# Performance work log

Measured on AMD Instinct MI355X. Metric: run time of the kernel, lower is better.

The kernel has to match this reference:

```python
import jax, jax.numpy as jnp
import numpy as np

# ---- P4M (D4) group: 8 elements, idx = 4*m + r (m: mirror bit, r: rot90 count) ----
G = 8

def _mr(i):
    return i // 4, i % 4

def _gidx(m, r):
    return 4 * (m % 2) + (r % 4)

def _comp(a, b):
    m1, r1 = _mr(a); m2, r2 = _mr(b)
    return _gidx(m1 + m2, (r1 if m2 == 0 else -r1) + r2)

_INV = [next(b for b in range(G) if _comp(a, b) == 0) for a in range(G)]
# _PERM[h, g] = index of h^{-1} * g  (left regular action on the group axis)
_PERM = np.array([[_comp(_INV[h], g) for g in range(G)] for h in range(G)])


def _spatial_transform(K, h):
    # act on the last two (spatial) kernel axes by group element h = mirror^m rot^r
    m, r = _mr(h)
    if m:
        K = jnp.flip(K, axis=-1)
    return jnp.rot90(K, k=r, axes=(-2, -1))


def _transformed_kernels(W):
    # W: [N_out, N_in, G, k, k] -> [G, N_out, N_in, G, k, k], one kernel per output group element
    return jnp.stack([_spatial_transform(W[:, :, _PERM[h]], h) for h in range(G)])


def conv_gg(x, W, padding):
    # group->group convolution. x: [B, N_in, G, H, W]; W: [N_out, N_in, G, k, k]
    B, Ni, _, H, Wd = x.shape
    No, k = W.shape[0], W.shape[-1]
    K = _transformed_kernels(W).reshape(G * No, Ni * G, k, k)
    y = jax.lax.conv_general_dilated(
        x.reshape(B, Ni * G, H, Wd), K, window_strides=(1, 1),
        padding=[(padding, padding), (padding, padding)],
        dimension_numbers=('NCHW', 'OIHW', 'NCHW'))
    Ho, Wo = y.shape[-2], y.shape[-1]
    return y.reshape(B, G, No, Ho, Wo).transpose(0, 2, 1, 3, 4)  # [B, N_out, G, Ho, Wo]


def channel_att_gg(x, W1, W2):
    # squeeze-excite over (channel, group) with group-equivariant weight sharing
    s = x.mean(axis=(-2, -1))                                  # [B, C, G]
    P1 = W1[:, :, _PERM]                                       # [M, C, G_out, G_in]
    t = jax.nn.relu(jnp.einsum('mcog,bcg->bmo', P1, s))        # [B, M, G]
    P2 = W2[:, :, _PERM]                                       # [C, M, G_out, G_in]
    return jax.nn.sigmoid(jnp.einsum('cmog,bmg->bco', P2, t))  # [B, C, G]


def spatial_att_gg(x, Wsp):
    # CBAM-style: mean/max over channels, group-equivariant 7x7 conv, sigmoid
    p = jnp.stack([x.mean(axis=1), x.max(axis=1)], axis=1)     # [B, 2, G, H, W]
    return jax.nn.sigmoid(conv_gg(p, Wsp, padding=Wsp.shape[-1] // 2))  # [B, 1, G, H, W]


def f_att_conv_gg(x, W, Wc1, Wc2, Wsp, padding):
    a_ch = channel_att_gg(x, Wc1, Wc2)[:, :, :, None, None]
    a_sp = spatial_att_gg(x, Wsp)
    return conv_gg(x * a_ch * a_sp, W, padding)


def bn3d(x, gamma, beta, eps=2e-5):
    # training-mode BatchNorm3d: stats over (B, G, H, W) per channel, biased variance
    mu = x.mean(axis=(0, 2, 3, 4), keepdims=True)
    var = ((x - mu) ** 2).mean(axis=(0, 2, 3, 4), keepdims=True)
    return (x - mu) * jax.lax.rsqrt(var + eps) * gamma[None, :, None, None, None] \
        + beta[None, :, None, None, None]


C, MID, K, SPK, B, H = 96, 48, 3, 7, 4, 56  # MID = C // ratio-reduction (ratio = C//2)


def setup_inputs() -> dict:
    key = jax.random.key(0)
    ks = jax.random.split(key, 12)
    def rn(k, shape, scale):
        return jax.random.normal(k, shape, dtype=jnp.float32) * scale
    wsc = float(np.sqrt(2.0 / (C * G * K * K)))
    asc = float(np.sqrt(2.0 / (C * G)))
    ssc = float(np.sqrt(2.0 / (2 * G * SPK * SPK)))
    return {
        'x': rn(ks[0], (B, C, G, H, H), 1.0),
        'bn1_gamma': jnp.ones((C,), jnp.float32), 'bn1_beta': jnp.zeros((C,), jnp.float32),
        'bn2_gamma': jnp.ones((C,), jnp.float32), 'bn2_beta': jnp.zeros((C,), jnp.float32),
        'c1_W': rn(ks[1], (C, C, G, K, K), wsc),
        'c1_att1': rn(ks[2], (MID, C, G), asc), 'c1_att2': rn(ks[3], (C, MID, G), asc),
        'c1_sp': rn(ks[4], (1, 2, G, SPK, SPK), ssc),
        'c2_W': rn(ks[5], (C, C, G, K, K), wsc),
        'c2_att1': rn(ks[6], (MID, C, G), asc), 'c2_att2': rn(ks[7], (C, MID, G), asc),
        'c2_sp': rn(ks[8], (1, 2, G, SPK, SPK), ssc),
    }


def reference(x, bn1_gamma, bn1_beta, bn2_gamma, bn2_beta,
              c1_W, c1_att1, c1_att2, c1_sp,
              c2_W, c2_att1, c2_att2, c2_sp):
    # fiber_map='id', stride=1 -> no group pooling, identity shortcut
    h = f_att_conv_gg(jax.nn.relu(bn3d(x, bn1_gamma, bn1_beta)),
                      c1_W, c1_att1, c1_att2, c1_sp, padding=1)
    h = f_att_conv_gg(jax.nn.relu(bn3d(h, bn2_gamma, bn2_beta)),
                      c2_W, c2_att1, c2_att2, c2_sp, padding=1)
    return x + h
```

## Files before the change

### kernel.cpp

```cpp
#include <hip/hip_runtime.h>
#include <math.h>

#define NG 8
#define C96 96
#define NMID 48
#define HW 56
#define PIX 3136
#define GHW 25088
#define CIN 768
#define NPIXT 9633792
#define BN_N 100352
#define PADW 58
#define PADPIX 3364
#define WTK 589824
#define PPL 3968

typedef __attribute__((ext_vector_type(8))) short bf16x8;
typedef __attribute__((ext_vector_type(4))) float f32x4;

__device__ __forceinline__ int d_comp(int a, int b){
  int m1=a>>2, r1=a&3, m2=b>>2, r2=b&3;
  int m=(m1+m2)&1;
  int r = (m2==0) ? (r1+r2) : (r2-r1);
  r = (r+4)&3;
  return 4*m+r;
}
__device__ __forceinline__ int d_inv(int a){ return (a>>2) ? a : ((4-(a&3))&3); }
__device__ __forceinline__ int d_perm(int h, int g){ return d_comp(d_inv(h), g); }

__device__ __forceinline__ void d_src(int h, int dy, int dx, int n, int* sy, int* sx){
  int r=h&3, m=h>>2, e=n-1;
  int y,x;
  if(r==0){y=dy; x=dx;}
  else if(r==1){y=dx; x=e-dy;}
  else if(r==2){y=e-dy; x=e-dx;}
  else {y=e-dx; x=dy;}
  if(m) x = e-x;
  *sy=y; *sx=x;
}

__device__ __forceinline__ unsigned short f2bf(float f){
  unsigned int u = __builtin_bit_cast(unsigned int, f);
  unsigned int r = (u + 0x7FFFu + ((u>>16)&1u)) >> 16;
  return (unsigned short)r;
}

__device__ __forceinline__ void gload_lds16(const void* g, void* l){
  __builtin_amdgcn_global_load_lds((const __attribute__((address_space(1))) unsigned int*)g,
                                   (__attribute__((address_space(3))) unsigned int*)l, 16, 0, 0);
}

#define VMCNT6() do { asm volatile("s_waitcnt vmcnt(6)" ::: "memory"); \
                      __builtin_amdgcn_sched_barrier(0); } while(0)
#define VMCNT0() do { asm volatile("s_waitcnt vmcnt(0)" ::: "memory"); \
                      __builtin_amdgcn_sched_barrier(0); } while(0)
#define BAR() do { __builtin_amdgcn_s_barrier(); __builtin_amdgcn_sched_barrier(0); } while(0)

__global__ void k_bn_stats(const float* __restrict__ in, float* __restrict__ spart){
  __shared__ float sm[8];
  int c = blockIdx.x, s = blockIdx.y;
  int b = s>>1, half = s&1;
  const float4* p = (const float4*)(in + ((size_t)(b*C96 + c))*GHW) + half*(GHW/8);
  float sum=0.f, sum2=0.f;
  for (int i=threadIdx.x; i<GHW/8; i+=256){
    float4 v = p[i];
    sum  += v.x+v.y+v.z+v.w;
    sum2 += v.x*v.x+v.y*v.y+v.z*v.z+v.w*v.w;
  }
  #pragma unroll
  for (int off=32; off>0; off>>=1){ sum += __shfl_down(sum,off); sum2 += __shfl_down(sum2,off); }
  int lane=threadIdx.x&63, wid=threadIdx.x>>6;
  if(lane==0){ sm[wid]=sum; sm[4+wid]=sum2; }
  __syncthreads();
  if(threadIdx.x==0){
    float a=sm[0]+sm[1]+sm[2]+sm[3], b2=sm[4]+sm[5]+sm[6]+sm[7];
    spart[(c*8+s)*2]   = a;
    spart[(c*8+s)*2+1] = b2;
  }
}

__global__ __launch_bounds__(256) void k_pool(const float* __restrict__ in,
    const float* __restrict__ spart, const float* __restrict__ gamma, const float* __restrict__ beta,
    float* __restrict__ pp){
  __shared__ float scs[C96], shs[C96];
  int tid = threadIdx.x;
  if (tid < C96){
    float s=0.f, s2=0.f;
    #pragma unroll
    for (int k=0;k<8;k++){ s += spart[(tid*8+k)*2]; s2 += spart[(tid*8+k)*2+1]; }
    float mean = s*(1.f/BN_N);
    float var  = s2*(1.f/BN_N) - mean*mean;
    float sc = gamma[tid]*rsqrtf(var + 2e-5f);
    scs[tid] = sc; shs[tid] = beta[tid] - mean*sc;
  }
  __syncthreads();
  int bg = blockIdx.y; int b = bg>>3, g = bg&7;
  int px = blockIdx.x*256 + tid;
  if (px >= PIX) return;
  float pm = 0.f, pmx = 0.f;
  for (int c = 0; c < C96; c++){
    size_t idx = ((size_t)((b*C96 + c)*8 + g))*PIX + px;
    float v = fmaxf(fmaf(in[idx], scs[c], shs[c]), 0.f);
    pm += v; pmx = fmaxf(pmx, v);
  }
  int y = px/HW, x = px - y*HW;
  pp[(size_t)(b*16 + g)*PPL     + (y+3)*64 + (x+3)] = pm;
  pp[(size_t)(b*16 + 8 + g)*PPL + (y+3)*64 + (x+3)] = pmx;
}

__global__ void k_chan(const float* __restrict__ in, const float* __restrict__ spart,
    const float* __restrict__ gamma, const float* __restrict__ beta, float* __restrict__ sout){
  int bcg = blockIdx.x;
  int c = (bcg >> 3) % C96;
  float s=0.f, s2=0.f;
  #pragma unroll
  for (int k=0;k<8;k++){ s += spart[(c*8+k)*2]; s2 += spart[(c*8+k)*2+1]; }
  float mean = s*(1.f/BN_N);
  float var  = s2*(1.f/BN_N) - mean*mean;
  float sc = gamma[c]*rsqrtf(var + 2e-5f);
  float sh = beta[c] - mean*sc;
  const float4* p = (const float4*)(in + (size_t)bcg*PIX);
  float acc=0.f;
  for (int i=threadIdx.x; i<PIX/4; i+=64){
    float4 v = p[i];
    acc += fmaxf(fmaf(v.x,sc,sh),0.f) + fmaxf(fmaf(v.y,sc,sh),0.f)
         + fmaxf(fmaf(v.z,sc,sh),0.f) + fmaxf(fmaf(v.w,sc,sh),0.f);
  }
  #pragma unroll
  for(int off=32;off>0;off>>=1) acc += __shfl_down(acc,off);
  if(threadIdx.x==0) sout[bcg] = acc * (1.f/3136.f);
}

__global__ void k_ca(const float* __restrict__ sbuf, const float* __restrict__ W1,
                     const float* __restrict__ W2, float* __restrict__ ach){
  __shared__ float sl[CIN], tl[NMID*8];
  int b = blockIdx.x, tid = threadIdx.x;
  sl[tid] = sbuf[b*CIN + tid];
  __syncthreads();
  int o = tid & 7;
  int pg[8];
  #pragma unroll
  for (int g=0; g<8; g++) pg[g] = d_perm(o, g);
  if (tid < NMID*8){
    int m = tid >> 3;
    float acc = 0.f;
    for (int c=0; c<C96; c++){
      #pragma unroll
      for (int g=0; g<8; g++) acc += W1[(m*C96+c)*8+pg[g]] * sl[c*8+g];
    }
    tl[tid] = fmaxf(acc, 0.f);
  }
  __syncthreads();
  {
    int c = tid >> 3;
    float acc = 0.f;
    for (int m=0; m<NMID; m++){
      #pragma unroll
      for (int g=0; g<8; g++) acc += W2[(c*NMID+m)*8+pg[g]] * tl[(m<<3)+g];
    }
    ach[b*CIN + tid] = 1.f/(1.f+__expf(-acc));
  }
}

__global__ __launch_bounds__(256) void k_sp_conv(const float* __restrict__ pp,
    const float* __restrict__ Wsp, float* __restrict__ aspt){
  __shared__ float wl[2*8*49];
  int bh = blockIdx.y; int b=bh>>3, h=bh&7;
  for(int idx=threadIdx.x; idx<784; idx+=256){
    int i = idx/392; int rem = idx-i*392;
    int g = rem/49; int kk = rem-g*49;
    int dy=kk/7, dx=kk-dy*7;
    int pg = d_perm(h,g);
    int sy,sx; d_src(h,dy,dx,7,&sy,&sx);
    wl[idx] = Wsp[(i*8+pg)*49 + sy*7+sx] * (i==0 ? (1.f/96.f) : 1.f);
  }
  __syncthreads();
  int pix = blockIdx.x*256 + threadIdx.x;
  if(pix>=PIX) return;
  int y=pix/HW, x=pix-y*HW;
  const float* base = pp + (size_t)(b*16)*PPL + y*64 + x;
  float acc=0.f;
  for(int ig=0; ig<16; ig++){
    const float* pb = base + (size_t)ig*PPL;
    const float* wb = wl + ig*49;
    #pragma unroll
    for(int dy=0; dy<7; dy++){
      #pragma unroll
      for(int dx=0; dx<7; dx++)
        acc = fmaf(pb[dy*64+dx], wb[dy*7+dx], acc);
    }
  }
  aspt[((size_t)b*PIX + pix)*8 + h] = 1.f/(1.f+__expf(-acc));
}

__global__ void k_zerob(uint4* __restrict__ xp, uint4* __restrict__ pp){
  uint4 z = (uint4){0u,0u,0u,0u};
  int i = blockIdx.x*256 + threadIdx.x;
  if (blockIdx.x < 248){ pp[i] = z; return; }
  int r = i - 63488;
  if (r >= 87552) return;
  int b = r / 21888;
  int q = r - b*21888;
  int p = q / 96, j = q - p*96;
  int y, x;
  if (p < 58){ y=0; x=p; }
  else if (p < 116){ y=57; x=p-58; }
  else if (p < 172){ y=p-115; x=0; }
  else { y=p-171; x=57; }
  xp[(size_t)(b*PADPIX + y*PADW + x)*96 + j] = z;
}

__global__ __launch_bounds__(256) void k_mod_t(const float* __restrict__ in,
    const float* __restrict__ spart, const float* __restrict__ gamma, const float* __restrict__ beta,
    const float* __restrict__ ach, const float* __restrict__ aspt,
    unsigned int* __restrict__ XpU){
  __shared__ float tile[64][65];
  __shared__ float scs8[8], shs8[8];
  int b = blockIdx.z;
  int cg0 = blockIdx.y*64;
  int pix0 = blockIdx.x*64;
  int tid = threadIdx.x;
  if (tid < 8){
    int c = (cg0>>3) + tid;
    float s=0.f, s2=0.f;
    #pragma unroll
    for (int k=0;k<8;k++){ s += spart[(c*8+k)*2]; s2 += spart[(c*8+k)*2+1]; }
    float mean = s*(1.f/BN_N);
    float var  = s2*(1.f/BN_N) - mean*mean;
    float sc = gamma[c]*rsqrtf(var + 2e-5f);
    scs8[tid] = sc; shs8[tid] = beta[c] - mean*sc;
  }
  __syncthreads();
  int lane = tid & 63, w = tid >> 6;
  for (int r = w; r < 64; r += 4){
    int cg = cg0 + r;
    float a1 = ach[b*CIN + cg];
    float raw = in[(size_t)(b*CIN + cg)*PIX + pix0 + lane];
    float v = fmaxf(fmaf(raw, scs8[r>>3], shs8[r>>3]), 0.f);
    tile[r][lane] = v * a1;
  }
  __syncthreads();
  int half = lane >> 5;
  int cgA = (lane & 31)*2;
  #pragma unroll
  for (int it = 0; it < 8; it++){
    int p = it*8 + w*2 + half;
    int pix = pix0 + p;
    int y = pix/HW, x = pix - y*HW;
    float2 a2 = *(const float2*)(aspt + ((size_t)b*PIX + pix)*8 + (cgA&7));
    float vA = tile[cgA][p]   * a2.x;
    float vB = tile[cgA+1][p] * a2.y;
    unsigned int u = (unsigned int)f2bf(vA) | ((unsigned int)f2bf(vB) << 16);
    XpU[(((size_t)b*PADPIX + (y+1)*PADW + (x+1))*CIN + cg0 + cgA) >> 1] = u;
  }
}

__global__ void k_ktb2(const float* __restrict__ W1src, const float* __restrict__ W2src,
                       unsigned short* __restrict__ Wt1, unsigned short* __restrict__ Wt2){
  const float* W = blockIdx.y ? W2src : W1src;
  unsigned short* Wt = blockIdx.y ? Wt2 : Wt1;
  int idx = blockIdx.x*256 + threadIdx.x;
  int ci = idx % CIN;
  int t2 = idx / CIN;
  int co = t2 % CIN;
  int kk = t2 / CIN;
  int h = co/C96, o = co - h*C96;
  int i = ci >> 3, g = ci & 7;
  int dy = kk/3, dx = kk - dy*3;
  int sy, sx; d_src(h, dy, dx, 3, &sy, &sx);
  float v = W[((o*C96 + i)*8 + d_perm(h,g))*9 + sy*3 + sx];
  Wt[idx] = f2bf(v);
}

__global__ __launch_bounds__(256, 2) void k_convmf(const unsigned short* __restrict__ Xp,
    const unsigned short* __restrict__ Wt, const float* __restrict__ resid,
    float* __restrict__ out){
  __shared__ unsigned short lds[40960];
  int tid = threadIdx.x, lane = tid & 63, w = tid >> 6;
  int col = lane & 15, kg = lane >> 4;

  int bid = blockIdx.x;
  int wgid = (bid & 7)*56 + (bid >> 3);
  int m = wgid/112; int rem = wgid - m*112;
  int b = rem/28;  int rp = rem - b*28;
  int y0 = rp*2, co0 = m*192;

  int xgo[8], xds[8];
  #pragma unroll
  for (int t = 0; t < 8; t++){
    int fg = (w*8 + t)*64 + lane;
    int row = fg >> 9;
    int pr  = (fg >> 3) & 63;
    int gi  = fg & 7;
    int sg  = gi ^ (pr & 7);
    xgo[t] = (b*PADPIX + (y0+row)*PADW + pr)*CIN + sg*8;
    xds[t] = (w*8 + t)*512;
  }
  int wgo[6], wofs[6];
  {
    int crow = lane >> 3, gi = lane & 7, sg = gi ^ crow;
    #pragma unroll
    for (int j = 0; j < 6; j++){
      int cb = w*48 + j*8;
      wgo[j]  = (co0 + cb + crow)*CIN + sg*8;
      wofs[j] = cb*64;
    }
  }
  int aidx[3][2];
  #pragma unroll
  for (int mf = 0; mf < 3; mf++)
    #pragma unroll
    for (int ks = 0; ks < 2; ks++)
      aidx[mf][ks] = (w*48 + mf*16 + col)*64 + ((((ks<<2)|kg) ^ (col&7)) << 3);

  int boff[3][7];
  #pragma unroll
  for (int nf=0; nf<7; nf++){
    int q2 = nf*16 + col;
    int qyl = (q2 >= 56) ? 1 : 0;
    int qx = q2 - 56*qyl;
    #pragma unroll
    for (int dx=0; dx<3; dx++){
      int t1 = qx + dx;
      boff[dx][nf] = (qyl<<12) | (t1<<6) | ((kg ^ (t1&7))<<3);
    }
  }

  f32x4 acc[3][7];
  #pragma unroll
  for (int mf=0; mf<3; mf++)
    #pragma unroll
    for (int nf=0; nf<7; nf++)
      acc[mf][nf] = (f32x4){0.f,0.f,0.f,0.f};

  #pragma unroll
  for (int j = 0; j < 6; j++) gload_lds16(Wt + wgo[j], &lds[16384 + wofs[j]]);
  #pragma unroll
  for (int t = 0; t < 8; t++) gload_lds16(Xp + xgo[t], &lds[xds[t]]);
  VMCNT0();
  BAR();

  int q = 0;
  for (int chunk = 0; chunk < 12; chunk++){
    int ci0 = chunk << 6;
    #pragma unroll
    for (int kk = 0; kk < 9; kk++){
      int s = chunk*9 + kk;
      if (s <= 106){
        int kk2 = kk + 1, c2 = chunk;
        if (kk2 == 9){ kk2 = 0; c2++; }
        size_t gofs = (size_t)kk2*WTK + (c2 << 6);
        int dofs = 16384 + (q^1)*12288;
        #pragma unroll
        for (int j = 0; j < 6; j++) gload_lds16(Wt + gofs + wgo[j], &lds[dofs + wofs[j]]);
        VMCNT6();
      } else {
        VMCNT0();
      }
      const unsigned short* Wb = &lds[16384 + q*12288];
      bf16x8 A00 = *(const bf16x8*)(Wb + aidx[0][0]);
      bf16x8 A01 = *(const bf16x8*)(Wb + aidx[0][1]);
      bf16x8 A10 = *(const bf16x8*)(Wb + aidx[1][0]);
      bf16x8 A11 = *(const bf16x8*)(Wb + aidx[1][1]);
      bf16x8 A20 = *(const bf16x8*)(Wb + aidx[2][0]);
      bf16x8 A21 = *(const bf16x8*)(Wb + aidx[2][1]);
      int dyk = kk/3, dxk = kk - dyk*3;
      const int dyo = dyk << 12;
      __builtin_amdgcn_s_setprio(1);
      #pragma unroll
      for (int nf = 0; nf < 7; nf++){
        bf16x8 B0 = *(const bf16x8*)(lds + boff[dxk][nf] + dyo);
        bf16x8 B1 = *(const bf16x8*)(lds + ((boff[dxk][nf] + dyo) ^ 32));
        acc[0][nf] = __builtin_amdgcn_mfma_f32_16x16x32_bf16(A00, B0, acc[0][nf], 0,0,0);
        acc[1][nf] = __builtin_amdgcn_mfma_f32_16x16x32_bf16(A10, B0, acc[1][nf], 0,0,0);
        acc[2][nf] = __builtin_amdgcn_mfma_f32_16x16x32_bf16(A20, B0, acc[2][nf], 0,0,0);
        acc[0][nf] = __builtin_amdgcn_mfma_f32_16x16x32_bf16(A01, B1, acc[0][nf], 0,0,0);
        acc[1][nf] = __builtin_amdgcn_mfma_f32_16x16x32_bf16(A11, B1, acc[1][nf], 0,0,0);
        acc[2][nf] = __builtin_amdgcn_mfma_f32_16x16x32_bf16(A21, B1, acc[2][nf], 0,0,0);
      }
      __builtin_amdgcn_s_setprio(0);
      q ^= 1;
      if (kk == 8 && chunk < 11){
        BAR();
        #pragma unroll
        for (int t = 0; t < 8; t++) gload_lds16(Xp + xgo[t] + ci0 + 64, &lds[xds[t]]);
        VMCNT0();
        BAR();
      }
    }
  }

  #pragma unroll
  for (int mf = 0; mf < 3; mf++){
    int co_b = co0 + w*48 + mf*16;
    int h = co_b/C96;
    int ob = co_b - h*C96 + kg*4;
    #pragma unroll
    for (int nf = 0; nf < 7; nf++){
      int qq = nf*16 + col;
      #pragma unroll
      for (int r = 0; r < 4; r++){
        size_t oi = ((size_t)((b*C96 + ob + r)*8 + h))*PIX + y0*56 + qq;
        float v = acc[mf][nf][r];
        if (resid) v += resid[oi];
        out[oi] = v;
      }
    }
  }
}

static void run_layer(const float* bn_in,
                      const float* a1W, const float* a2W, const float* spW,
                      const float* bng, const float* bnb,
                      const float* resid, float* convout,
                      float* spart, float* sbuf, float* ach, float* ppP, float* aspt,
                      unsigned short* Wt, unsigned short* Xp, hipStream_t stream)
{
  k_bn_stats<<<dim3(C96,8),256,0,stream>>>(bn_in, spart);
  k_pool<<<dim3(13,32),256,0,stream>>>(bn_in, spart, bng, bnb, ppP);
  k_chan<<<4*C96*NG,64,0,stream>>>(bn_in, spart, bng, bnb, sbuf);
  k_ca<<<4,CIN,0,stream>>>(sbuf, a1W, a2W, ach);
  k_sp_conv<<<dim3(13,32),256,0,stream>>>(ppP, spW, aspt);
  k_mod_t<<<dim3(PIX/64, CIN/64, 4),256,0,stream>>>(bn_in, spart, bng, bnb, ach, aspt, (unsigned int*)Xp);
  k_convmf<<<448,256,0,stream>>>(Xp, Wt, resid, convout);
}

extern "C" void kernel_launch(void* const* d_in, const int* in_sizes, int n_in,
                              void* d_out, int out_size, void* d_ws, size_t ws_size,
                              hipStream_t stream) {
  const float* x    = (const float*)d_in[0];
  const float* bn1g = (const float*)d_in[1];
  const float* bn1b = (const float*)d_in[2];
  const float* bn2g = (const float*)d_in[3];
  const float* bn2b = (const float*)d_in[4];
  const float* c1W  = (const float*)d_in[5];
  const float* c1a1 = (const float*)d_in[6];
  const float* c1a2 = (const float*)d_in[7];
  const float* c1sp = (const float*)d_in[8];
  const float* c2W  = (const float*)d_in[9];
  const float* c2a1 = (const float*)d_in[10];
  const float* c2a2 = (const float*)d_in[11];
  const float* c2sp = (const float*)d_in[12];
  float* out = (float*)d_out;
  float* ws  = (float*)d_ws;

  float* bufA = ws;
  unsigned short* Wt1 = (unsigned short*)(bufA + NPIXT);
  unsigned short* Wt2 = Wt1 + 9*CIN*CIN;
  unsigned short* Xp  = Wt2 + 9*CIN*CIN;
  float* spart = (float*)(Xp + (size_t)4*PADPIX*CIN);
  float* sbuf  = spart + 1536;
  float* ach   = sbuf + 4*C96*NG;
  float* ppP   = ach + 4*C96*NG;
  float* aspt  = ppP + 4*16*PPL;

  k_ktb2<<<dim3((9*CIN*CIN)/256, 2),256,0,stream>>>(c1W, c2W, Wt1, Wt2);
  k_zerob<<<590,256,0,stream>>>((uint4*)Xp, (uint4*)ppP);

  run_layer(x, c1a1, c1a2, c1sp, bn1g, bn1b, nullptr, bufA,
            spart, sbuf, ach, ppP, aspt, Wt1, Xp, stream);
  run_layer(bufA, c2a1, c2a2, c2sp, bn2g, bn2b, x, out,
            spart, sbuf, ach, ppP, aspt, Wt2, Xp, stream);
}
```

Measured before the change: 543.5 us.

## Fuse channel-mean pooling into spatial pool kernel via atomics; hoist MFMA B loads

Removes the separate k_chan kernel, which re-read the full activation tensor to compute per-(b,c,g) spatial means. The k_pool kernel (renamed k_pc) now does a wave-level shuffle reduction for every channel and atomically adds the partial sums into sbuf. k_bn_stats zeroes sbuf first, and k_ca applies the 1/3136 scaling. Separately, the conv kernel loads all 14 B fragments from LDS before the MFMA loop so that LDS reads can overlap with the matrix work, at the cost of more registers. The per-channel shuffle reduction adds ALU work inside the pooling loop, and the atomics make the summation order nondeterministic.

```diff
diff --git a/kernel.cpp b/kernel.cpp
--- a/kernel.cpp
+++ b/kernel.cpp
@@ -56,10 +56,12 @@
                       __builtin_amdgcn_sched_barrier(0); } while(0)
 #define BAR() do { __builtin_amdgcn_s_barrier(); __builtin_amdgcn_sched_barrier(0); } while(0)
 
-__global__ void k_bn_stats(const float* __restrict__ in, float* __restrict__ spart){
+__global__ void k_bn_stats(const float* __restrict__ in, float* __restrict__ spart,
+                           float* __restrict__ sbuf){
   __shared__ float sm[8];
   int c = blockIdx.x, s = blockIdx.y;
   int b = s>>1, half = s&1;
+  if (threadIdx.x < 4) sbuf[((b*C96 + c)<<3) + ((s&1)<<2) + threadIdx.x] = 0.f;
   const float4* p = (const float4*)(in + ((size_t)(b*C96 + c))*GHW) + half*(GHW/8);
   float sum=0.f, sum2=0.f;
   for (int i=threadIdx.x; i<GHW/8; i+=256){
@@ -79,9 +81,9 @@
   }
 }
 
-__global__ __launch_bounds__(256) void k_pool(const float* __restrict__ in,
+__global__ __launch_bounds__(256) void k_pc(const float* __restrict__ in,
     const float* __restrict__ spart, const float* __restrict__ gamma, const float* __restrict__ beta,
-    float* __restrict__ pp){
+    float* __restrict__ pp, float* __restrict__ sbuf){
   __shared__ float scs[C96], shs[C96];
   int tid = threadIdx.x;
   if (tid < C96){
@@ -97,45 +99,27 @@
   int bg = blockIdx.y; int b = bg>>3, g = bg&7;
   int px = blockIdx.x*256 + tid;
   if (px >= PIX) return;
+  int lane = tid & 63;
   float pm = 0.f, pmx = 0.f;
   for (int c = 0; c < C96; c++){
     size_t idx = ((size_t)((b*C96 + c)*8 + g))*PIX + px;
     float v = fmaxf(fmaf(in[idx], scs[c], shs[c]), 0.f);
     pm += v; pmx = fmaxf(pmx, v);
+    float r = v;
+    #pragma unroll
+    for (int off=32; off>0; off>>=1) r += __shfl_down(r, off);
+    if (lane == 0) atomicAdd(&sbuf[(b*C96 + c)*8 + g], r);
   }
   int y = px/HW, x = px - y*HW;
   pp[(size_t)(b*16 + g)*PPL     + (y+3)*64 + (x+3)] = pm;
   pp[(size_t)(b*16 + 8 + g)*PPL + (y+3)*64 + (x+3)] = pmx;
-}
-
-__global__ void k_chan(const float* __restrict__ in, const float* __restrict__ spart,
-    const float* __restrict__ gamma, const float* __restrict__ beta, float* __restrict__ sout){
-  int bcg = blockIdx.x;
-  int c = (bcg >> 3) % C96;
-  float s=0.f, s2=0.f;
-  #pragma unroll
-  for (int k=0;k<8;k++){ s += spart[(c*8+k)*2]; s2 += spart[(c*8+k)*2+1]; }
-  float mean = s*(1.f/BN_N);
-  float var  = s2*(1.f/BN_N) - mean*mean;
-  float sc = gamma[c]*rsqrtf(var + 2e-5f);
-  float sh = beta[c] - mean*sc;
-  const float4* p = (const float4*)(in + (size_t)bcg*PIX);
-  float acc=0.f;
-  for (int i=threadIdx.x; i<PIX/4; i+=64){
-    float4 v = p[i];
-    acc += fmaxf(fmaf(v.x,sc,sh),0.f) + fmaxf(fmaf(v.y,sc,sh),0.f)
-         + fmaxf(fmaf(v.z,sc,sh),0.f) + fmaxf(fmaf(v.w,sc,sh),0.f);
-  }
-  #pragma unroll
-  for(int off=32;off>0;off>>=1) acc += __shfl_down(acc,off);
-  if(threadIdx.x==0) sout[bcg] = acc * (1.f/3136.f);
 }
 
 __global__ void k_ca(const float* __restrict__ sbuf, const float* __restrict__ W1,
                      const float* __restrict__ W2, float* __restrict__ ach){
   __shared__ float sl[CIN], tl[NMID*8];
   int b = blockIdx.x, tid = threadIdx.x;
-  sl[tid] = sbuf[b*CIN + tid];
+  sl[tid] = sbuf[b*CIN + tid] * (1.f/3136.f);
   __syncthreads();
   int o = tid & 7;
   int pg[8];
@@ -306,12 +290,12 @@
       wofs[j] = cb*64;
     }
   }
-  int aidx[3][2];
+  int aidx[6];
   #pragma unroll
   for (int mf = 0; mf < 3; mf++)
     #pragma unroll
     for (int ks = 0; ks < 2; ks++)
-      aidx[mf][ks] = (w*48 + mf*16 + col)*64 + ((((ks<<2)|kg) ^ (col&7)) << 3);
+      aidx[mf*2+ks] = (w*48 + mf*16 + col)*64 + ((((ks<<2)|kg) ^ (col&7)) << 3);
 
   int boff[3][7];
   #pragma unroll
@@ -358,25 +342,27 @@
         VMCNT0();
       }
       const unsigned short* Wb = &lds[16384 + q*12288];
-      bf16x8 A00 = *(const bf16x8*)(Wb + aidx[0][0]);
-      bf16x8 A01 = *(const bf16x8*)(Wb + aidx[0][1]);
-      bf16x8 A10 = *(const bf16x8*)(Wb + aidx[1][0]);
-      bf16x8 A11 = *(const bf16x8*)(Wb + aidx[1][1]);
-      bf16x8 A20 = *(const bf16x8*)(Wb + aidx[2][0]);
-      bf16x8 A21 = *(const bf16x8*)(Wb + aidx[2][1]);
-      int dyk = kk/3, dxk = kk - dyk*3;
+      bf16x8 Af[6];
+      #pragma unroll
+      for (int i = 0; i < 6; i++) Af[i] = *(const bf16x8*)(Wb + aidx[i]);
+      const int dyk = kk/3, dxk = kk - dyk*3;
       const int dyo = dyk << 12;
+      bf16x8 Bv[14];
+      #pragma unroll
+      for (int nf = 0; nf < 7; nf++){
+        int base = boff[dxk][nf] + dyo;
+        Bv[2*nf]   = *(const bf16x8*)(lds + base);
+        Bv[2*nf+1] = *(const bf16x8*)(lds + (base ^ 32));
+      }
       __builtin_amdgcn_s_setprio(1);
       #pragma unroll
       for (int nf = 0; nf < 7; nf++){
-        bf16x8 B0 = *(const bf16x8*)(lds + boff[dxk][nf] + dyo);
-        bf16x8 B1 = *(const bf16x8*)(lds + ((boff[dxk][nf] + dyo) ^ 32));
-        acc[0][nf] = __builtin_amdgcn_mfma_f32_16x16x32_bf16(A00, B0, acc[0][nf], 0,0,0);
-        acc[1][nf] = __builtin_amdgcn_mfma_f32_16x16x32_bf16(A10, B0, acc[1][nf], 0,0,0);
-        acc[2][nf] = __builtin_amdgcn_mfma_f32_16x16x32_bf16(A20, B0, acc[2][nf], 0,0,0);
-        acc[0][nf] = __builtin_amdgcn_mfma_f32_16x16x32_bf16(A01, B1, acc[0][nf], 0,0,0);
-        acc[1][nf] = __builtin_amdgcn_mfma_f32_16x16x32_bf16(A11, B1, acc[1][nf], 0,0,0);
-        acc[2][nf] = __builtin_amdgcn_mfma_f32_16x16x32_bf16(A21, B1, acc[2][nf], 0,0,0);
+        acc[0][nf] = __builtin_amdgcn_mfma_f32_16x16x32_bf16(Af[0], Bv[2*nf],   acc[0][nf], 0,0,0);
+        acc[1][nf] = __builtin_amdgcn_mfma_f32_16x16x32_bf16(Af[2], Bv[2*nf],   acc[1][nf], 0,0,0);
+        acc[2][nf] = __builtin_amdgcn_mfma_f32_16x16x32_bf16(Af[4], Bv[2*nf],   acc[2][nf], 0,0,0);
+        acc[0][nf] = __builtin_amdgcn_mfma_f32_16x16x32_bf16(Af[1], Bv[2*nf+1], acc[0][nf], 0,0,0);
+        acc[1][nf] = __builtin_amdgcn_mfma_f32_16x16x32_bf16(Af[3], Bv[2*nf+1], acc[1][nf], 0,0,0);
+        acc[2][nf] = __builtin_amdgcn_mfma_f32_16x16x32_bf16(Af[5], Bv[2*nf+1], acc[2][nf], 0,0,0);
       }
       __builtin_amdgcn_s_setprio(0);
       q ^= 1;
@@ -416,9 +402,8 @@
                       float* spart, float* sbuf, float* ach, float* ppP, float* aspt,
                       unsigned short* Wt, unsigned short* Xp, hipStream_t stream)
 {
-  k_bn_stats<<<dim3(C96,8),256,0,stream>>>(bn_in, spart);
-  k_pool<<<dim3(13,32),256,0,stream>>>(bn_in, spart, bng, bnb, ppP);
-  k_chan<<<4*C96*NG,64,0,stream>>>(bn_in, spart, bng, bnb, sbuf);
+  k_bn_stats<<<dim3(C96,8),256,0,stream>>>(bn_in, spart, sbuf);
+  k_pc<<<dim3(13,32),256,0,stream>>>(bn_in, spart, bng, bnb, ppP, sbuf);
   k_ca<<<4,CIN,0,stream>>>(sbuf, a1W, a2W, ach);
   k_sp_conv<<<dim3(13,32),256,0,stream>>>(ppP, spW, aspt);
   k_mod_t<<<dim3(PIX/64, CIN/64, 4),256,0,stream>>>(bn_in, spart, bng, bnb, ach, aspt, (unsigned int*)Xp);
```

Measured after the change: 757.5 us. 39.4% more time.

## Retile grouped conv GEMM to smaller tiles for higher occupancy

Applied to the files above, without the earlier changes.

The MFMA conv kernel shrinks its output-channel tile from 192 to 128 and its K chunk from 64 to 32 channels. Shared memory per block drops so four blocks can share a compute unit instead of two, and the grid grows to 672 blocks. The XOR swizzle on the LDS layouts is removed in favour of plain linear addressing. The aim is more waves and better latency hiding, at the cost of twice as many chunk barriers, less operand reuse per LDS read, and possible bank conflicts from the unswizzled layout.

```diff
diff --git a/kernel.cpp b/kernel.cpp
--- a/kernel.cpp
+++ b/kernel.cpp
@@ -50,7 +50,7 @@
                                    (__attribute__((address_space(3))) unsigned int*)l, 16, 0, 0);
 }
 
-#define VMCNT6() do { asm volatile("s_waitcnt vmcnt(6)" ::: "memory"); \
+#define VMCNT2() do { asm volatile("s_waitcnt vmcnt(2)" ::: "memory"); \
                       __builtin_amdgcn_sched_barrier(0); } while(0)
 #define VMCNT0() do { asm volatile("s_waitcnt vmcnt(0)" ::: "memory"); \
                       __builtin_amdgcn_sched_barrier(0); } while(0)
@@ -272,118 +272,98 @@
   Wt[idx] = f2bf(v);
 }
 
-__global__ __launch_bounds__(256, 2) void k_convmf(const unsigned short* __restrict__ Xp,
+__global__ __launch_bounds__(256, 4) void k_convmf(const unsigned short* __restrict__ Xp,
     const unsigned short* __restrict__ Wt, const float* __restrict__ resid,
     float* __restrict__ out){
-  __shared__ unsigned short lds[40960];
+  __shared__ unsigned short lds[16384];
+  char* ldsb = (char*)lds;
   int tid = threadIdx.x, lane = tid & 63, w = tid >> 6;
   int col = lane & 15, kg = lane >> 4;
 
   int bid = blockIdx.x;
-  int wgid = (bid & 7)*56 + (bid >> 3);
+  int wgid = (bid & 7)*84 + (bid >> 3);
   int m = wgid/112; int rem = wgid - m*112;
   int b = rem/28;  int rp = rem - b*28;
-  int y0 = rp*2, co0 = m*192;
-
-  int xgo[8], xds[8];
-  #pragma unroll
-  for (int t = 0; t < 8; t++){
-    int fg = (w*8 + t)*64 + lane;
-    int row = fg >> 9;
-    int pr  = (fg >> 3) & 63;
-    int gi  = fg & 7;
-    int sg  = gi ^ (pr & 7);
-    xgo[t] = (b*PADPIX + (y0+row)*PADW + pr)*CIN + sg*8;
-    xds[t] = (w*8 + t)*512;
-  }
-  int wgo[6], wofs[6];
-  {
-    int crow = lane >> 3, gi = lane & 7, sg = gi ^ crow;
-    #pragma unroll
-    for (int j = 0; j < 6; j++){
-      int cb = w*48 + j*8;
-      wgo[j]  = (co0 + cb + crow)*CIN + sg*8;
-      wofs[j] = cb*64;
-    }
-  }
-  int aidx[3][2];
-  #pragma unroll
-  for (int mf = 0; mf < 3; mf++)
-    #pragma unroll
-    for (int ks = 0; ks < 2; ks++)
-      aidx[mf][ks] = (w*48 + mf*16 + col)*64 + ((((ks<<2)|kg) ^ (col&7)) << 3);
-
-  int boff[3][7];
+  int y0 = rp*2, co0 = m*128;
+
+  int xgo[4], xds[4];
+  #pragma unroll
+  for (int t = 0; t < 4; t++){
+    int slot = t*256 + tid;
+    int row = slot >> 8;
+    int px  = (slot >> 2) & 63;
+    int g   = slot & 3;
+    xgo[t] = (b*PADPIX + (y0+row)*PADW + px)*CIN + g*8;
+    xds[t] = slot*16;
+  }
+  int wgo[2], wds[2];
+  #pragma unroll
+  for (int j = 0; j < 2; j++){
+    wgo[j] = (co0 + w*32 + j*16 + (lane>>2))*CIN + (lane&3)*8;
+    wds[j] = 16384 + (w*32 + j*16)*64 + lane*16;
+  }
+  int awo[2];
+  #pragma unroll
+  for (int mf = 0; mf < 2; mf++)
+    awo[mf] = 16384 + (w*32 + mf*16 + col)*64 + kg*16;
+  int bb[7];
   #pragma unroll
   for (int nf=0; nf<7; nf++){
     int q2 = nf*16 + col;
     int qyl = (q2 >= 56) ? 1 : 0;
     int qx = q2 - 56*qyl;
-    #pragma unroll
-    for (int dx=0; dx<3; dx++){
-      int t1 = qx + dx;
-      boff[dx][nf] = (qyl<<12) | (t1<<6) | ((kg ^ (t1&7))<<3);
-    }
-  }
-
-  f32x4 acc[3][7];
-  #pragma unroll
-  for (int mf=0; mf<3; mf++)
+    bb[nf] = qyl*4096 + qx*64 + kg*16;
+  }
+
+  f32x4 acc[2][7];
+  #pragma unroll
+  for (int mf=0; mf<2; mf++)
     #pragma unroll
     for (int nf=0; nf<7; nf++)
       acc[mf][nf] = (f32x4){0.f,0.f,0.f,0.f};
 
   #pragma unroll
-  for (int j = 0; j < 6; j++) gload_lds16(Wt + wgo[j], &lds[16384 + wofs[j]]);
-  #pragma unroll
-  for (int t = 0; t < 8; t++) gload_lds16(Xp + xgo[t], &lds[xds[t]]);
+  for (int j = 0; j < 2; j++) gload_lds16(Wt + wgo[j], ldsb + wds[j]);
+  #pragma unroll
+  for (int t = 0; t < 4; t++) gload_lds16(Xp + xgo[t], ldsb + xds[t]);
   VMCNT0();
   BAR();
 
   int q = 0;
-  for (int chunk = 0; chunk < 12; chunk++){
-    int ci0 = chunk << 6;
+  for (int chunk = 0; chunk < 24; chunk++){
+    int ci0 = chunk << 5;
     #pragma unroll
     for (int kk = 0; kk < 9; kk++){
       int s = chunk*9 + kk;
-      if (s <= 106){
-        int kk2 = kk + 1, c2 = chunk;
-        if (kk2 == 9){ kk2 = 0; c2++; }
-        size_t gofs = (size_t)kk2*WTK + (c2 << 6);
-        int dofs = 16384 + (q^1)*12288;
+      if (s < 215){
+        int kk2 = (kk == 8) ? 0 : kk+1;
+        int c2  = (kk == 8) ? chunk+1 : chunk;
+        size_t gofs = (size_t)kk2*WTK + (c2 << 5);
+        int dofs = (q^1)*8192;
         #pragma unroll
-        for (int j = 0; j < 6; j++) gload_lds16(Wt + gofs + wgo[j], &lds[dofs + wofs[j]]);
-        VMCNT6();
+        for (int j = 0; j < 2; j++) gload_lds16(Wt + gofs + wgo[j], ldsb + dofs + wds[j]);
+        VMCNT2();
       } else {
         VMCNT0();
       }
-      const unsigned short* Wb = &lds[16384 + q*12288];
-      bf16x8 A00 = *(const bf16x8*)(Wb + aidx[0][0]);
-      bf16x8 A01 = *(const bf16x8*)(Wb + aidx[0][1]);
-      bf16x8 A10 = *(const bf16x8*)(Wb + aidx[1][0]);
-      bf16x8 A11 = *(const bf16x8*)(Wb + aidx[1][1]);
-      bf16x8 A20 = *(const bf16x8*)(Wb + aidx[2][0]);
-      bf16x8 A21 = *(const bf16x8*)(Wb + aidx[2][1]);
-      int dyk = kk/3, dxk = kk - dyk*3;
-      const int dyo = dyk << 12;
+      const int wq = q*8192;
+      bf16x8 A0 = *(const bf16x8*)(ldsb + awo[0] + wq);
+      bf16x8 A1 = *(const bf16x8*)(ldsb + awo[1] + wq);
+      const int dyk = kk/3, dxk = kk - dyk*3;
+      const int dofs2 = dyk*4096 + dxk*64;
       __builtin_amdgcn_s_setprio(1);
       #pragma unroll
       for (int nf = 0; nf < 7; nf++){
-        bf16x8 B0 = *(const bf16x8*)(lds + boff[dxk][nf] + dyo);
-        bf16x8 B1 = *(const bf16x8*)(lds + ((boff[dxk][nf] + dyo) ^ 32));
-        acc[0][nf] = __builtin_amdgcn_mfma_f32_16x16x32_bf16(A00, B0, acc[0][nf], 0,0,0);
-        acc[1][nf] = __builtin_amdgcn_mfma_f32_16x16x32_bf16(A10, B0, acc[1][nf], 0,0,0);
-        acc[2][nf] = __builtin_amdgcn_mfma_f32_16x16x32_bf16(A20, B0, acc[2][nf], 0,0,0);
-        acc[0][nf] = __builtin_amdgcn_mfma_f32_16x16x32_bf16(A01, B1, acc[0][nf], 0,0,0);
-        acc[1][nf] = __builtin_amdgcn_mfma_f32_16x16x32_bf16(A11, B1, acc[1][nf], 0,0,0);
-        acc[2][nf] = __builtin_amdgcn_mfma_f32_16x16x32_bf16(A21, B1, acc[2][nf], 0,0,0);
+        bf16x8 B = *(const bf16x8*)(ldsb + bb[nf] + dofs2);
+        acc[0][nf] = __builtin_amdgcn_mfma_f32_16x16x32_bf16(A0, B, acc[0][nf], 0,0,0);
+        acc[1][nf] = __builtin_amdgcn_mfma_f32_16x16x32_bf16(A1, B, acc[1][nf], 0,0,0);
       }
       __builtin_amdgcn_s_setprio(0);
       q ^= 1;
-      if (kk == 8 && chunk < 11){
+      if (kk == 8 && chunk < 23){
         BAR();
         #pragma unroll
-        for (int t = 0; t < 8; t++) gload_lds16(Xp + xgo[t] + ci0 + 64, &lds[xds[t]]);
+        for (int t = 0; t < 4; t++) gload_lds16(Xp + xgo[t] + ci0 + 32, ldsb + xds[t]);
         VMCNT0();
         BAR();
       }
@@ -391,8 +371,8 @@
   }
 
   #pragma unroll
-  for (int mf = 0; mf < 3; mf++){
-    int co_b = co0 + w*48 + mf*16;
+  for (int mf = 0; mf < 2; mf++){
+    int co_b = co0 + w*32 + mf*16;
     int h = co_b/C96;
     int ob = co_b - h*C96 + kg*4;
     #pragma unroll
@@ -422,7 +402,7 @@
   k_ca<<<4,CIN,0,stream>>>(sbuf, a1W, a2W, ach);
   k_sp_conv<<<dim3(13,32),256,0,stream>>>(ppP, spW, aspt);
   k_mod_t<<<dim3(PIX/64, CIN/64, 4),256,0,stream>>>(bn_in, spart, bng, bnb, ach, aspt, (unsigned int*)Xp);
-  k_convmf<<<448,256,0,stream>>>(Xp, Wt, resid, convout);
+  k_convmf<<<672,256,0,stream>>>(Xp, Wt, resid, convout);
 }
 
 extern "C" void kernel_launch(void* const* d_in, const int* in_sizes, int n_in,
```

New measurement: 543.0 us. About the same (-0.1%).
